# Optimization experiments

Hardware: AMD Instinct MI355X
Metric: run time of the kernel (lower is better)

The kernel has to match this reference:

```python
import math
import jax, jax.numpy as jnp
import numpy as np

DIM = 1024
N_HEADS = 16
N_KV_HEADS = 4
HEAD_DIM = 64
WINDOW = 512
EPS = 1e-6
B, S = 2, 2048

def _alibi_slopes(n_heads):
    def pow2(n):
        r = 2.0 ** (-8.0 / n)
        return np.array([r ** (i + 1) for i in range(n)], dtype=np.float32)
    if math.log2(n_heads).is_integer():
        return pow2(n_heads)
    m = 2 ** math.floor(math.log2(n_heads))
    return np.concatenate([pow2(m), pow2(2 * m)[::2][: n_heads - m]])

def _rmsnorm(x, w, eps=EPS):
    var = jnp.mean(x * x, axis=-1, keepdims=True)
    return x * jax.lax.rsqrt(var + eps) * w

def setup_inputs() -> dict:
    key = jax.random.key(0)
    ks = jax.random.split(key, 8)
    x = jax.random.normal(ks[0], (B, S, DIM), dtype=jnp.float32)
    wq = 0.02 * jax.random.normal(ks[1], (N_HEADS * HEAD_DIM, DIM), dtype=jnp.float32)
    wk = 0.02 * jax.random.normal(ks[2], (N_KV_HEADS * HEAD_DIM, DIM), dtype=jnp.float32)
    wv = 0.02 * jax.random.normal(ks[3], (N_KV_HEADS * HEAD_DIM, DIM), dtype=jnp.float32)
    wo = 0.02 * jax.random.normal(ks[4], (DIM, N_HEADS * HEAD_DIM), dtype=jnp.float32)
    q_norm_w = jnp.ones((N_HEADS * HEAD_DIM,), dtype=jnp.float32)
    k_norm_w = jnp.ones((N_KV_HEADS * HEAD_DIM,), dtype=jnp.float32)
    return {"x": x, "wq": wq, "wk": wk, "wv": wv, "wo": wo,
            "q_norm_w": q_norm_w, "k_norm_w": k_norm_w}

def reference(x, wq, wk, wv, wo, q_norm_w, k_norm_w):
    bsz, seqlen, _ = x.shape
    repeats = N_HEADS // N_KV_HEADS
    xq = _rmsnorm(x @ wq.T, q_norm_w)
    xk = _rmsnorm(x @ wk.T, k_norm_w)
    xv = x @ wv.T
    # [b, h, s, d]
    q = xq.reshape(bsz, seqlen, N_HEADS, HEAD_DIM).transpose(0, 2, 1, 3)
    k = xk.reshape(bsz, seqlen, N_KV_HEADS, HEAD_DIM).transpose(0, 2, 1, 3)
    v = xv.reshape(bsz, seqlen, N_KV_HEADS, HEAD_DIM).transpose(0, 2, 1, 3)
    k = jnp.repeat(k, repeats, axis=1)
    v = jnp.repeat(v, repeats, axis=1)
    pos = jnp.arange(seqlen)
    rel = pos[None, :] - pos[:, None]  # [s_q, s_k], key - query
    slopes = jnp.asarray(_alibi_slopes(N_HEADS))
    bias = slopes[:, None, None] * rel[None].astype(x.dtype)  # [h, s, s]
    masked = (rel > 0) | (rel < -WINDOW)  # causal + sliding window
    bias = jnp.where(masked[None], -jnp.inf, bias)
    scale = 1.0 / math.sqrt(HEAD_DIM)
    scores = jnp.einsum('bhqd,bhkd->bhqk', q, k) * scale + bias[None]
    probs = jax.nn.softmax(scores, axis=-1)
    y = jnp.einsum('bhqk,bhkd->bhqd', probs, v)
    y = y.transpose(0, 2, 1, 3).reshape(bsz, seqlen, N_HEADS * HEAD_DIM)
    return y @ wo.T
```

## Files before the change

kernel.cpp:

```cpp
#include <hip/hip_runtime.h>

typedef unsigned short u16;
typedef unsigned int u32;

typedef __bf16 bf16x8 __attribute__((ext_vector_type(8)));
typedef float f32x4 __attribute__((ext_vector_type(4)));

__device__ __forceinline__ u16 f2bf(float f) {
  u32 u = __builtin_bit_cast(u32, f);
  u32 r = (u + 0x7fffu + ((u >> 16) & 1u)) >> 16;
  return (u16)r;
}
__device__ __forceinline__ float bf2f(u16 v) {
  u32 u = (u32)v << 16;
  return __builtin_bit_cast(float, u);
}

typedef const __attribute__((address_space(1))) void* gas_ptr;
typedef __attribute__((address_space(3))) void* las_ptr;
__device__ __forceinline__ void gl2lds16(const void* g, void* l) {
  __builtin_amdgcn_global_load_lds((gas_ptr)g, (las_ptr)l, 16, 0, 0);
}

__global__ __launch_bounds__(256)
void cvt_all_kernel(const float* __restrict__ x, const float* __restrict__ wq,
                    const float* __restrict__ wk, const float* __restrict__ wv,
                    const float* __restrict__ wo, u16* __restrict__ x_bf,
                    u16* __restrict__ wcat_bf, u16* __restrict__ wo_bf) {
  int t = blockIdx.x * 256 + threadIdx.x;
  const float* src;
  u16* dst;
  if (t < 1048576) {
    src = x; dst = x_bf;
  } else if (t < 1310720) {
    src = wq; dst = wcat_bf; t -= 1048576;
  } else if (t < 1376256) {
    src = wk; dst = wcat_bf + 1048576; t -= 1310720;
  } else if (t < 1441792) {
    src = wv; dst = wcat_bf + 1310720; t -= 1376256;
  } else {
    src = wo; dst = wo_bf; t -= 1441792;
  }
  const int i = t * 4;
  float4 v = *(const float4*)(src + i);
  uint2 p;
  p.x = (u32)f2bf(v.x) | ((u32)f2bf(v.y) << 16);
  p.y = (u32)f2bf(v.z) | ((u32)f2bf(v.w) << 16);
  *(uint2*)(dst + i) = p;
}

template <typename OutT>
__global__ __launch_bounds__(256)
void gemm_bt_kernel(const u16* __restrict__ A, const u16* __restrict__ B,
                    OutT* __restrict__ C, int M, int N, int K) {
  __shared__ u16 As[128 * 32];
  __shared__ u16 Bs[128 * 32];
  const int tid = threadIdx.x;
  const int lane = tid & 63;
  const int wave = tid >> 6;
  const int wm = (wave >> 1) * 64;
  const int wn = (wave & 1) * 64;
  const int l15 = lane & 15;
  const int qk = (lane >> 4) * 8;
  const size_t bm = (size_t)blockIdx.y * 128;
  const size_t bn = (size_t)blockIdx.x * 128;

  f32x4 acc[4][4];
#pragma unroll
  for (int i = 0; i < 4; ++i)
#pragma unroll
    for (int j = 0; j < 4; ++j) acc[i][j] = f32x4{0.f, 0.f, 0.f, 0.f};

  const int r0 = tid >> 2;
  const int c0 = (tid & 3) * 8;
  const u16* Ab = A + (bm + r0) * (size_t)K + c0;
  const u16* Bb = B + (bn + r0) * (size_t)K + c0;
  const int wbase = wave * 512;

  for (int k0 = 0; k0 < K; k0 += 32) {
    __syncthreads();
    gl2lds16(Ab + k0, &As[wbase]);
    gl2lds16(Ab + (size_t)64 * K + k0, &As[2048 + wbase]);
    gl2lds16(Bb + k0, &Bs[wbase]);
    gl2lds16(Bb + (size_t)64 * K + k0, &Bs[2048 + wbase]);
    __syncthreads();
    bf16x8 af[4], bfr[4];
#pragma unroll
    for (int i = 0; i < 4; ++i)
      af[i] = *(const bf16x8*)(&As[(wm + i * 16 + l15) * 32 + qk]);
#pragma unroll
    for (int j = 0; j < 4; ++j)
      bfr[j] = *(const bf16x8*)(&Bs[(wn + j * 16 + l15) * 32 + qk]);
#pragma unroll
    for (int i = 0; i < 4; ++i)
#pragma unroll
      for (int j = 0; j < 4; ++j)
        acc[i][j] = __builtin_amdgcn_mfma_f32_16x16x32_bf16(af[i], bfr[j], acc[i][j], 0, 0, 0);
  }

  const int rq = (lane >> 4) * 4;
#pragma unroll
  for (int i = 0; i < 4; ++i) {
#pragma unroll
    for (int r = 0; r < 4; ++r) {
      OutT* crow = C + (bm + wm + i * 16 + rq + r) * (size_t)N + bn + wn + l15;
#pragma unroll
      for (int j = 0; j < 4; ++j) {
        if constexpr (sizeof(OutT) == 2)
          crow[j * 16] = f2bf(acc[i][j][r]);
        else
          crow[j * 16] = acc[i][j][r];
      }
    }
  }
}

__global__ __launch_bounds__(256)
void rmsnorm_kernel(u16* __restrict__ qkv, const float* __restrict__ qw,
                    const float* __restrict__ kw) {
  __shared__ float red[4];
  const int tid = threadIdx.x;
  u16* row = qkv + (size_t)blockIdx.x * 1536;
  uint2 pk = *(const uint2*)(row + tid * 4);
  float v0 = bf2f((u16)pk.x), v1 = bf2f((u16)(pk.x >> 16));
  float v2 = bf2f((u16)pk.y), v3 = bf2f((u16)(pk.y >> 16));
  float ss = v0 * v0 + v1 * v1 + v2 * v2 + v3 * v3;
#pragma unroll
  for (int off = 32; off > 0; off >>= 1) ss += __shfl_down(ss, off);
  if ((tid & 63) == 0) red[tid >> 6] = ss;
  __syncthreads();
  float tot = red[0] + red[1] + red[2] + red[3];
  float rn = rsqrtf(tot * (1.0f / 1024.0f) + 1e-6f);
  float4 w = *(const float4*)(qw + tid * 4);
  uint2 po;
  po.x = (u32)f2bf(v0 * rn * w.x) | ((u32)f2bf(v1 * rn * w.y) << 16);
  po.y = (u32)f2bf(v2 * rn * w.z) | ((u32)f2bf(v3 * rn * w.w) << 16);
  *(uint2*)(row + tid * 4) = po;
  if (tid < 64) {
    uint2 kp = *(const uint2*)(row + 1024 + tid * 4);
    float k0 = bf2f((u16)kp.x), k1 = bf2f((u16)(kp.x >> 16));
    float k2 = bf2f((u16)kp.y), k3 = bf2f((u16)(kp.y >> 16));
    float sk = k0 * k0 + k1 * k1 + k2 * k2 + k3 * k3;
#pragma unroll
    for (int off = 32; off > 0; off >>= 1) sk += __shfl_down(sk, off);
    float tk = __shfl(sk, 0);
    float rk = rsqrtf(tk * (1.0f / 256.0f) + 1e-6f);
    float4 w2 = *(const float4*)(kw + tid * 4);
    uint2 ko;
    ko.x = (u32)f2bf(k0 * rk * w2.x) | ((u32)f2bf(k1 * rk * w2.y) << 16);
    ko.y = (u32)f2bf(k2 * rk * w2.z) | ((u32)f2bf(k3 * rk * w2.w) << 16);
    *(uint2*)(row + 1024 + tid * 4) = ko;
  }
}

__global__ __launch_bounds__(256)
void vtrans_kernel(const u16* __restrict__ qkv, u16* __restrict__ vt) {
  __shared__ u16 tile[64][72];
  const int tid = threadIdx.x;
  const int t0 = blockIdx.x * 64, kvh = blockIdx.y, b = blockIdx.z;
  const int r = tid >> 2, c16 = (tid & 3) * 16;
  const u16* src = qkv + (size_t)(b * 2048 + t0 + r) * 1536 + 1280 + kvh * 64 + c16;
  *(uint4*)&tile[r][c16] = *(const uint4*)src;
  *(uint4*)&tile[r][c16 + 8] = *(const uint4*)(src + 8);
  __syncthreads();
  const int d = tid >> 2, t16 = (tid & 3) * 16;
  u16 o[16];
#pragma unroll
  for (int j = 0; j < 16; ++j) o[j] = tile[t16 + j][d];
  u16* dst = vt + (size_t)((b * 4 + kvh) * 64 + d) * 2048 + t0 + t16;
  *(uint4*)dst = *(uint4*)&o[0];
  *(uint4*)(dst + 8) = *(uint4*)&o[8];
}

__global__ __launch_bounds__(256)
void attn_kernel(const u16* __restrict__ qkvbf, const u16* __restrict__ vt,
                 u16* __restrict__ ybf) {
  __shared__ u16 Ks[64 * 72];
  __shared__ u16 Vts[64 * 72];
  __shared__ u16 Ps[64 * 72];
  const int qt = blockIdx.x, h = blockIdx.y, b = blockIdx.z;
  const int kvh = h >> 2, q0 = qt * 64;
  const int tid = threadIdx.x, lane = tid & 63, w = tid >> 6;
  const int l15 = lane & 15, quad = lane >> 4;

  const u16* qrow = qkvbf + (size_t)(b * 2048 + q0 + w * 16 + l15) * 1536 + h * 64 + quad * 8;
  const bf16x8 qf0 = *(const bf16x8*)qrow;
  const bf16x8 qf1 = *(const bf16x8*)(qrow + 32);

  const int sr = tid >> 2, sc = (tid & 3) * 16;
  const u16* kbase = qkvbf + (size_t)(b * 2048 + sr) * 1536 + 1024 + kvh * 64 + sc;
  const u16* vbase = vt + (size_t)((b * 4 + kvh) * 64 + sr) * 2048 + sc;

  f32x4 O[4];
#pragma unroll
  for (int jd = 0; jd < 4; ++jd) O[jd] = f32x4{0.f, 0.f, 0.f, 0.f};
  float m_i = -1e30f, l_i = 0.f;
  const float slope = exp2f(-0.5f * (float)(h + 1));
  const int c_lo = (q0 >= 512) ? (q0 - 512) : 0;
  const int myq = q0 + w * 16 + l15;

  for (int c = c_lo; c <= q0; c += 64) {
    __syncthreads();
    {
      const u16* kp = kbase + (size_t)c * 1536;
      const u16* vp = vbase + c;
      uint4 ka = *(const uint4*)kp, kb = *(const uint4*)(kp + 8);
      uint4 va = *(const uint4*)vp, vb = *(const uint4*)(vp + 8);
      *(uint4*)&Ks[sr * 72 + sc] = ka;
      *(uint4*)&Ks[sr * 72 + sc + 8] = kb;
      *(uint4*)&Vts[sr * 72 + sc] = va;
      *(uint4*)&Vts[sr * 72 + sc + 8] = vb;
    }
    __syncthreads();

    f32x4 st[4];
#pragma unroll
    for (int i = 0; i < 4; ++i) {
      bf16x8 a0 = *(const bf16x8*)&Ks[(i * 16 + l15) * 72 + quad * 8];
      bf16x8 a1 = *(const bf16x8*)&Ks[(i * 16 + l15) * 72 + 32 + quad * 8];
      f32x4 z = f32x4{0.f, 0.f, 0.f, 0.f};
      z = __builtin_amdgcn_mfma_f32_16x16x32_bf16(a0, qf0, z, 0, 0, 0);
      st[i] = __builtin_amdgcn_mfma_f32_16x16x32_bf16(a1, qf1, z, 0, 0, 0);
    }

    float sv[4][4];
    float rm = -1e30f;
#pragma unroll
    for (int i = 0; i < 4; ++i) {
#pragma unroll
      for (int r = 0; r < 4; ++r) {
        const int key = c + i * 16 + quad * 4 + r;
        const int rel = key - myq;
        float val = (rel > 0 || rel < -512) ? -1e30f
                                            : st[i][r] * 0.125f + slope * (float)rel;
        sv[i][r] = val;
        rm = fmaxf(rm, val);
      }
    }
    rm = fmaxf(rm, __shfl_xor(rm, 16));
    rm = fmaxf(rm, __shfl_xor(rm, 32));
    const float mn = fmaxf(m_i, rm);
    const float alpha = __expf(m_i - mn);
    float ls = 0.f;
#pragma unroll
    for (int i = 0; i < 4; ++i) {
      float p0 = __expf(sv[i][0] - mn);
      float p1 = __expf(sv[i][1] - mn);
      float p2 = __expf(sv[i][2] - mn);
      float p3 = __expf(sv[i][3] - mn);
      ls += (p0 + p1) + (p2 + p3);
      uint2 pw;
      pw.x = (u32)f2bf(p0) | ((u32)f2bf(p1) << 16);
      pw.y = (u32)f2bf(p2) | ((u32)f2bf(p3) << 16);
      *(uint2*)&Ps[(w * 16 + l15) * 72 + i * 16 + quad * 4] = pw;
    }
    ls += __shfl_xor(ls, 16);
    ls += __shfl_xor(ls, 32);
    l_i = l_i * alpha + ls;
    m_i = mn;

    float ar[4];
#pragma unroll
    for (int r = 0; r < 4; ++r) ar[r] = __shfl(alpha, quad * 4 + r);
#pragma unroll
    for (int jd = 0; jd < 4; ++jd)
#pragma unroll
      for (int r = 0; r < 4; ++r) O[jd][r] *= ar[r];

    __syncthreads();

    bf16x8 pf0 = *(const bf16x8*)&Ps[(w * 16 + l15) * 72 + quad * 8];
    bf16x8 pf1 = *(const bf16x8*)&Ps[(w * 16 + l15) * 72 + 32 + quad * 8];
#pragma unroll
    for (int jd = 0; jd < 4; ++jd) {
      bf16x8 v0 = *(const bf16x8*)&Vts[(jd * 16 + l15) * 72 + quad * 8];
      bf16x8 v1 = *(const bf16x8*)&Vts[(jd * 16 + l15) * 72 + 32 + quad * 8];
      O[jd] = __builtin_amdgcn_mfma_f32_16x16x32_bf16(pf0, v0, O[jd], 0, 0, 0);
      O[jd] = __builtin_amdgcn_mfma_f32_16x16x32_bf16(pf1, v1, O[jd], 0, 0, 0);
    }
  }

  float lr[4];
#pragma unroll
  for (int r = 0; r < 4; ++r) lr[r] = __shfl(l_i, quad * 4 + r);
#pragma unroll
  for (int r = 0; r < 4; ++r) {
    const float inv = 1.0f / lr[r];
    u16* orow = ybf + (size_t)(b * 2048 + q0 + w * 16 + quad * 4 + r) * 1024 + h * 64 + l15;
#pragma unroll
    for (int jd = 0; jd < 4; ++jd) orow[jd * 16] = f2bf(O[jd][r] * inv);
  }
}

extern "C" void kernel_launch(void* const* d_in, const int* in_sizes, int n_in,
                              void* d_out, int out_size, void* d_ws, size_t ws_size,
                              hipStream_t stream) {
  const float* x = (const float*)d_in[0];
  const float* wq = (const float*)d_in[1];
  const float* wk = (const float*)d_in[2];
  const float* wv = (const float*)d_in[3];
  const float* wo = (const float*)d_in[4];
  const float* qnw = (const float*)d_in[5];
  const float* knw = (const float*)d_in[6];
  float* out = (float*)d_out;
  char* ws = (char*)d_ws;

  u16* x_bf = (u16*)(ws);
  u16* wcat_bf = (u16*)(ws + 8388608);
  u16* wo_bf = (u16*)(ws + 11534336);
  u16* qkv_bf = (u16*)(ws + 13631488);
  u16* vt_bf = (u16*)(ws + 26214400);
  u16* y_bf = (u16*)(ws + 28311552);

  cvt_all_kernel<<<6656, 256, 0, stream>>>(x, wq, wk, wv, wo, x_bf, wcat_bf, wo_bf);

  gemm_bt_kernel<u16><<<dim3(12, 32), 256, 0, stream>>>(x_bf, wcat_bf, qkv_bf, 4096, 1536, 1024);
  rmsnorm_kernel<<<4096, 256, 0, stream>>>(qkv_bf, qnw, knw);
  vtrans_kernel<<<dim3(32, 4, 2), 256, 0, stream>>>(qkv_bf, vt_bf);
  attn_kernel<<<dim3(32, 16, 2), 256, 0, stream>>>(qkv_bf, vt_bf, y_bf);
  gemm_bt_kernel<float><<<dim3(8, 32), 256, 0, stream>>>(y_bf, wo_bf, out, 4096, 1024, 1024);
}
```

Measured before the change: 180.9 us.

## Prefetch tiles in GEMM and attention, fuse norm with V transpose, use exp2

```diff
diff --git a/kernel.cpp b/kernel.cpp
--- a/kernel.cpp
+++ b/kernel.cpp
@@ -14,12 +14,6 @@
 __device__ __forceinline__ float bf2f(u16 v) {
   u32 u = (u32)v << 16;
   return __builtin_bit_cast(float, u);
-}
-
-typedef const __attribute__((address_space(1))) void* gas_ptr;
-typedef __attribute__((address_space(3))) void* las_ptr;
-__device__ __forceinline__ void gl2lds16(const void* g, void* l) {
-  __builtin_amdgcn_global_load_lds((gas_ptr)g, (las_ptr)l, 16, 0, 0);
 }
 
 __global__ __launch_bounds__(256)
@@ -53,21 +47,21 @@
 __global__ __launch_bounds__(256)
 void gemm_bt_kernel(const u16* __restrict__ A, const u16* __restrict__ B,
                     OutT* __restrict__ C, int M, int N, int K) {
-  __shared__ u16 As[128 * 32];
+  __shared__ u16 As[64 * 32];
   __shared__ u16 Bs[128 * 32];
   const int tid = threadIdx.x;
   const int lane = tid & 63;
   const int wave = tid >> 6;
-  const int wm = (wave >> 1) * 64;
+  const int wm = (wave >> 1) * 32;
   const int wn = (wave & 1) * 64;
   const int l15 = lane & 15;
   const int qk = (lane >> 4) * 8;
-  const size_t bm = (size_t)blockIdx.y * 128;
+  const size_t bm = (size_t)blockIdx.y * 64;
   const size_t bn = (size_t)blockIdx.x * 128;
 
-  f32x4 acc[4][4];
-#pragma unroll
-  for (int i = 0; i < 4; ++i)
+  f32x4 acc[2][4];
+#pragma unroll
+  for (int i = 0; i < 2; ++i)
 #pragma unroll
     for (int j = 0; j < 4; ++j) acc[i][j] = f32x4{0.f, 0.f, 0.f, 0.f};
 
@@ -75,24 +69,30 @@
   const int c0 = (tid & 3) * 8;
   const u16* Ab = A + (bm + r0) * (size_t)K + c0;
   const u16* Bb = B + (bn + r0) * (size_t)K + c0;
-  const int wbase = wave * 512;
+
+  uint4 ar = *(const uint4*)(Ab);
+  uint4 br0 = *(const uint4*)(Bb);
+  uint4 br1 = *(const uint4*)(Bb + (size_t)64 * K);
 
   for (int k0 = 0; k0 < K; k0 += 32) {
     __syncthreads();
-    gl2lds16(Ab + k0, &As[wbase]);
-    gl2lds16(Ab + (size_t)64 * K + k0, &As[2048 + wbase]);
-    gl2lds16(Bb + k0, &Bs[wbase]);
-    gl2lds16(Bb + (size_t)64 * K + k0, &Bs[2048 + wbase]);
-    __syncthreads();
-    bf16x8 af[4], bfr[4];
-#pragma unroll
-    for (int i = 0; i < 4; ++i)
+    *(uint4*)(&As[tid * 8]) = ar;
+    *(uint4*)(&Bs[tid * 8]) = br0;
+    *(uint4*)(&Bs[tid * 8 + 2048]) = br1;
+    __syncthreads();
+    const int kn = (k0 + 32 < K) ? k0 + 32 : 0;
+    ar = *(const uint4*)(Ab + kn);
+    br0 = *(const uint4*)(Bb + kn);
+    br1 = *(const uint4*)(Bb + (size_t)64 * K + kn);
+    bf16x8 af[2], bfr[4];
+#pragma unroll
+    for (int i = 0; i < 2; ++i)
       af[i] = *(const bf16x8*)(&As[(wm + i * 16 + l15) * 32 + qk]);
 #pragma unroll
     for (int j = 0; j < 4; ++j)
       bfr[j] = *(const bf16x8*)(&Bs[(wn + j * 16 + l15) * 32 + qk]);
 #pragma unroll
-    for (int i = 0; i < 4; ++i)
+    for (int i = 0; i < 2; ++i)
 #pragma unroll
       for (int j = 0; j < 4; ++j)
         acc[i][j] = __builtin_amdgcn_mfma_f32_16x16x32_bf16(af[i], bfr[j], acc[i][j], 0, 0, 0);
@@ -100,7 +100,7 @@
 
   const int rq = (lane >> 4) * 4;
 #pragma unroll
-  for (int i = 0; i < 4; ++i) {
+  for (int i = 0; i < 2; ++i) {
 #pragma unroll
     for (int r = 0; r < 4; ++r) {
       OutT* crow = C + (bm + wm + i * 16 + rq + r) * (size_t)N + bn + wn + l15;
@@ -116,60 +116,61 @@
 }
 
 __global__ __launch_bounds__(256)
-void rmsnorm_kernel(u16* __restrict__ qkv, const float* __restrict__ qw,
-                    const float* __restrict__ kw) {
-  __shared__ float red[4];
+void norm_vtrans_kernel(u16* __restrict__ qkv, const float* __restrict__ qw,
+                        const float* __restrict__ kw, u16* __restrict__ vt) {
+  __shared__ u16 shmem[64 * 72];
+  const int bid = blockIdx.x;
   const int tid = threadIdx.x;
-  u16* row = qkv + (size_t)blockIdx.x * 1536;
-  uint2 pk = *(const uint2*)(row + tid * 4);
-  float v0 = bf2f((u16)pk.x), v1 = bf2f((u16)(pk.x >> 16));
-  float v2 = bf2f((u16)pk.y), v3 = bf2f((u16)(pk.y >> 16));
-  float ss = v0 * v0 + v1 * v1 + v2 * v2 + v3 * v3;
-#pragma unroll
-  for (int off = 32; off > 0; off >>= 1) ss += __shfl_down(ss, off);
-  if ((tid & 63) == 0) red[tid >> 6] = ss;
-  __syncthreads();
-  float tot = red[0] + red[1] + red[2] + red[3];
-  float rn = rsqrtf(tot * (1.0f / 1024.0f) + 1e-6f);
-  float4 w = *(const float4*)(qw + tid * 4);
-  uint2 po;
-  po.x = (u32)f2bf(v0 * rn * w.x) | ((u32)f2bf(v1 * rn * w.y) << 16);
-  po.y = (u32)f2bf(v2 * rn * w.z) | ((u32)f2bf(v3 * rn * w.w) << 16);
-  *(uint2*)(row + tid * 4) = po;
-  if (tid < 64) {
-    uint2 kp = *(const uint2*)(row + 1024 + tid * 4);
-    float k0 = bf2f((u16)kp.x), k1 = bf2f((u16)(kp.x >> 16));
-    float k2 = bf2f((u16)kp.y), k3 = bf2f((u16)(kp.y >> 16));
-    float sk = k0 * k0 + k1 * k1 + k2 * k2 + k3 * k3;
-#pragma unroll
-    for (int off = 32; off > 0; off >>= 1) sk += __shfl_down(sk, off);
-    float tk = __shfl(sk, 0);
-    float rk = rsqrtf(tk * (1.0f / 256.0f) + 1e-6f);
-    float4 w2 = *(const float4*)(kw + tid * 4);
-    uint2 ko;
-    ko.x = (u32)f2bf(k0 * rk * w2.x) | ((u32)f2bf(k1 * rk * w2.y) << 16);
-    ko.y = (u32)f2bf(k2 * rk * w2.z) | ((u32)f2bf(k3 * rk * w2.w) << 16);
-    *(uint2*)(row + 1024 + tid * 4) = ko;
-  }
-}
-
-__global__ __launch_bounds__(256)
-void vtrans_kernel(const u16* __restrict__ qkv, u16* __restrict__ vt) {
-  __shared__ u16 tile[64][72];
-  const int tid = threadIdx.x;
-  const int t0 = blockIdx.x * 64, kvh = blockIdx.y, b = blockIdx.z;
-  const int r = tid >> 2, c16 = (tid & 3) * 16;
-  const u16* src = qkv + (size_t)(b * 2048 + t0 + r) * 1536 + 1280 + kvh * 64 + c16;
-  *(uint4*)&tile[r][c16] = *(const uint4*)src;
-  *(uint4*)&tile[r][c16 + 8] = *(const uint4*)(src + 8);
-  __syncthreads();
-  const int d = tid >> 2, t16 = (tid & 3) * 16;
-  u16 o[16];
-#pragma unroll
-  for (int j = 0; j < 16; ++j) o[j] = tile[t16 + j][d];
-  u16* dst = vt + (size_t)((b * 4 + kvh) * 64 + d) * 2048 + t0 + t16;
-  *(uint4*)dst = *(uint4*)&o[0];
-  *(uint4*)(dst + 8) = *(uint4*)&o[8];
+  if (bid < 4096) {
+    float* red = (float*)shmem;
+    u16* row = qkv + (size_t)bid * 1536;
+    uint2 pk = *(const uint2*)(row + tid * 4);
+    float v0 = bf2f((u16)pk.x), v1 = bf2f((u16)(pk.x >> 16));
+    float v2 = bf2f((u16)pk.y), v3 = bf2f((u16)(pk.y >> 16));
+    float ss = v0 * v0 + v1 * v1 + v2 * v2 + v3 * v3;
+#pragma unroll
+    for (int off = 32; off > 0; off >>= 1) ss += __shfl_down(ss, off);
+    if ((tid & 63) == 0) red[tid >> 6] = ss;
+    __syncthreads();
+    float tot = red[0] + red[1] + red[2] + red[3];
+    float rn = rsqrtf(tot * (1.0f / 1024.0f) + 1e-6f);
+    float4 w = *(const float4*)(qw + tid * 4);
+    uint2 po;
+    po.x = (u32)f2bf(v0 * rn * w.x) | ((u32)f2bf(v1 * rn * w.y) << 16);
+    po.y = (u32)f2bf(v2 * rn * w.z) | ((u32)f2bf(v3 * rn * w.w) << 16);
+    *(uint2*)(row + tid * 4) = po;
+    if (tid < 64) {
+      uint2 kp = *(const uint2*)(row + 1024 + tid * 4);
+      float k0 = bf2f((u16)kp.x), k1 = bf2f((u16)(kp.x >> 16));
+      float k2 = bf2f((u16)kp.y), k3 = bf2f((u16)(kp.y >> 16));
+      float sk = k0 * k0 + k1 * k1 + k2 * k2 + k3 * k3;
+#pragma unroll
+      for (int off = 32; off > 0; off >>= 1) sk += __shfl_down(sk, off);
+      float tk = __shfl(sk, 0);
+      float rk = rsqrtf(tk * (1.0f / 256.0f) + 1e-6f);
+      float4 w2 = *(const float4*)(kw + tid * 4);
+      uint2 ko;
+      ko.x = (u32)f2bf(k0 * rk * w2.x) | ((u32)f2bf(k1 * rk * w2.y) << 16);
+      ko.y = (u32)f2bf(k2 * rk * w2.z) | ((u32)f2bf(k3 * rk * w2.w) << 16);
+      *(uint2*)(row + 1024 + tid * 4) = ko;
+    }
+  } else {
+    const int e = bid - 4096;
+    const int t0 = (e & 31) * 64, kvh = (e >> 5) & 3, b = e >> 7;
+    u16(*tile)[72] = (u16(*)[72])shmem;
+    const int r = tid >> 2, c16 = (tid & 3) * 16;
+    const u16* src = qkv + (size_t)(b * 2048 + t0 + r) * 1536 + 1280 + kvh * 64 + c16;
+    *(uint4*)&tile[r][c16] = *(const uint4*)src;
+    *(uint4*)&tile[r][c16 + 8] = *(const uint4*)(src + 8);
+    __syncthreads();
+    const int d = tid >> 2, t16 = (tid & 3) * 16;
+    u16 o[16];
+#pragma unroll
+    for (int j = 0; j < 16; ++j) o[j] = tile[t16 + j][d];
+    u16* dst = vt + (size_t)((b * 4 + kvh) * 64 + d) * 2048 + t0 + t16;
+    *(uint4*)dst = *(uint4*)&o[0];
+    *(uint4*)(dst + 8) = *(uint4*)&o[8];
+  }
 }
 
 __global__ __launch_bounds__(256)
@@ -195,23 +196,35 @@
 #pragma unroll
   for (int jd = 0; jd < 4; ++jd) O[jd] = f32x4{0.f, 0.f, 0.f, 0.f};
   float m_i = -1e30f, l_i = 0.f;
-  const float slope = exp2f(-0.5f * (float)(h + 1));
+  const float LOG2E = 1.44269504f;
+  const float sc2 = 0.125f * LOG2E;
+  const float slope2 = exp2f(-0.5f * (float)(h + 1)) * LOG2E;
   const int c_lo = (q0 >= 512) ? (q0 - 512) : 0;
   const int myq = q0 + w * 16 + l15;
+  const int myq_lo = q0 + w * 16;
+
+  uint4 kr0, kr1, vr0, vr1;
+  {
+    const u16* kp = kbase + (size_t)c_lo * 1536;
+    const u16* vp = vbase + c_lo;
+    kr0 = *(const uint4*)kp;  kr1 = *(const uint4*)(kp + 8);
+    vr0 = *(const uint4*)vp;  vr1 = *(const uint4*)(vp + 8);
+  }
 
   for (int c = c_lo; c <= q0; c += 64) {
     __syncthreads();
+    *(uint4*)&Ks[sr * 72 + sc] = kr0;
+    *(uint4*)&Ks[sr * 72 + sc + 8] = kr1;
+    *(uint4*)&Vts[sr * 72 + sc] = vr0;
+    *(uint4*)&Vts[sr * 72 + sc + 8] = vr1;
+    __syncthreads();
     {
-      const u16* kp = kbase + (size_t)c * 1536;
-      const u16* vp = vbase + c;
-      uint4 ka = *(const uint4*)kp, kb = *(const uint4*)(kp + 8);
-      uint4 va = *(const uint4*)vp, vb = *(const uint4*)(vp + 8);
-      *(uint4*)&Ks[sr * 72 + sc] = ka;
-      *(uint4*)&Ks[sr * 72 + sc + 8] = kb;
-      *(uint4*)&Vts[sr * 72 + sc] = va;
-      *(uint4*)&Vts[sr * 72 + sc + 8] = vb;
-    }
-    __syncthreads();
+      const int cn = (c + 64 <= q0) ? c + 64 : c_lo;
+      const u16* kp = kbase + (size_t)cn * 1536;
+      const u16* vp = vbase + cn;
+      kr0 = *(const uint4*)kp;  kr1 = *(const uint4*)(kp + 8);
+      vr0 = *(const uint4*)vp;  vr1 = *(const uint4*)(vp + 8);
+    }
 
     f32x4 st[4];
 #pragma unroll
@@ -225,29 +238,41 @@
 
     float sv[4][4];
     float rm = -1e30f;
-#pragma unroll
-    for (int i = 0; i < 4; ++i) {
-#pragma unroll
-      for (int r = 0; r < 4; ++r) {
-        const int key = c + i * 16 + quad * 4 + r;
-        const int rel = key - myq;
-        float val = (rel > 0 || rel < -512) ? -1e30f
-                                            : st[i][r] * 0.125f + slope * (float)rel;
-        sv[i][r] = val;
-        rm = fmaxf(rm, val);
-      }
+    const bool interior = (c + 63 <= myq_lo) && (c + 512 >= myq_lo + 15);
+    if (interior) {
+#pragma unroll
+      for (int i = 0; i < 4; ++i)
+#pragma unroll
+        for (int r = 0; r < 4; ++r) {
+          const int key = c + i * 16 + quad * 4 + r;
+          float val = st[i][r] * sc2 + slope2 * (float)(key - myq);
+          sv[i][r] = val;
+          rm = fmaxf(rm, val);
+        }
+    } else {
+#pragma unroll
+      for (int i = 0; i < 4; ++i)
+#pragma unroll
+        for (int r = 0; r < 4; ++r) {
+          const int key = c + i * 16 + quad * 4 + r;
+          const int rel = key - myq;
+          float val = (rel > 0 || rel < -512) ? -1e30f
+                                              : st[i][r] * sc2 + slope2 * (float)rel;
+          sv[i][r] = val;
+          rm = fmaxf(rm, val);
+        }
     }
     rm = fmaxf(rm, __shfl_xor(rm, 16));
     rm = fmaxf(rm, __shfl_xor(rm, 32));
     const float mn = fmaxf(m_i, rm);
-    const float alpha = __expf(m_i - mn);
+    const float alpha = exp2f(m_i - mn);
     float ls = 0.f;
 #pragma unroll
     for (int i = 0; i < 4; ++i) {
-      float p0 = __expf(sv[i][0] - mn);
-      float p1 = __expf(sv[i][1] - mn);
-      float p2 = __expf(sv[i][2] - mn);
-      float p3 = __expf(sv[i][3] - mn);
+      float p0 = exp2f(sv[i][0] - mn);
+      float p1 = exp2f(sv[i][1] - mn);
+      float p2 = exp2f(sv[i][2] - mn);
+      float p3 = exp2f(sv[i][3] - mn);
       ls += (p0 + p1) + (p2 + p3);
       uint2 pw;
       pw.x = (u32)f2bf(p0) | ((u32)f2bf(p1) << 16);
@@ -266,8 +291,6 @@
     for (int jd = 0; jd < 4; ++jd)
 #pragma unroll
       for (int r = 0; r < 4; ++r) O[jd][r] *= ar[r];
-
-    __syncthreads();
 
     bf16x8 pf0 = *(const bf16x8*)&Ps[(w * 16 + l15) * 72 + quad * 8];
     bf16x8 pf1 = *(const bf16x8*)&Ps[(w * 16 + l15) * 72 + 32 + quad * 8];
@@ -314,9 +337,8 @@
 
   cvt_all_kernel<<<6656, 256, 0, stream>>>(x, wq, wk, wv, wo, x_bf, wcat_bf, wo_bf);
 
-  gemm_bt_kernel<u16><<<dim3(12, 32), 256, 0, stream>>>(x_bf, wcat_bf, qkv_bf, 4096, 1536, 1024);
-  rmsnorm_kernel<<<4096, 256, 0, stream>>>(qkv_bf, qnw, knw);
-  vtrans_kernel<<<dim3(32, 4, 2), 256, 0, stream>>>(qkv_bf, vt_bf);
+  gemm_bt_kernel<u16><<<dim3(12, 64), 256, 0, stream>>>(x_bf, wcat_bf, qkv_bf, 4096, 1536, 1024);
+  norm_vtrans_kernel<<<4352, 256, 0, stream>>>(qkv_bf, qnw, knw, vt_bf);
   attn_kernel<<<dim3(32, 16, 2), 256, 0, stream>>>(qkv_bf, vt_bf, y_bf);
-  gemm_bt_kernel<float><<<dim3(8, 32), 256, 0, stream>>>(y_bf, wo_bf, out, 4096, 1024, 1024);
-}
+  gemm_bt_kernel<float><<<dim3(8, 64), 256, 0, stream>>>(y_bf, wo_bf, out, 4096, 1024, 1024);
+}
```

Measured after the change: 171.9 us. 1.05x faster.
